# Optimization experiments

Measured on AMD Instinct MI355X. Metric: run time of the kernel, lower is better.

The kernel has to match this reference:

```python
import jax, jax.numpy as jnp
import numpy as np

B, T, F = 8192, 200, 16
H = 32  # LSTM units
D = 60  # 6 * FREQUENCY


def setup_inputs() -> dict:
    key = jax.random.key(0)
    ks = jax.random.split(key, 5)
    s = 0.1
    return {
        "x": jax.random.normal(ks[0], (B, T, F), jnp.float32),
        "W": jax.random.normal(ks[1], (F, 4 * H), jnp.float32) * s,
        "U": jax.random.normal(ks[2], (H, 4 * H), jnp.float32) * s,
        "b": jnp.zeros((4 * H,), jnp.float32),
        "W1": jax.random.normal(ks[3], (H, D), jnp.float32) * s,
        "b1": jnp.zeros((D,), jnp.float32),
        "W2": jax.random.normal(ks[4], (H, D), jnp.float32) * s,
        "b2": jnp.zeros((D,), jnp.float32),
    }


def _lstm_last(x, W, U, b):
    # Precompute input-to-gate projections for all timesteps: [B, T, 4H]
    xg = jnp.einsum('btf,fg->btg', x, W) + b
    batch = x.shape[0]
    h0 = jnp.zeros((batch, H), x.dtype)
    c0 = jnp.zeros((batch, H), x.dtype)

    def step(carry, xg_t):
        h, c = carry
        g = xg_t + h @ U  # [B, 4H]
        i, f, cc, o = jnp.split(g, 4, axis=-1)  # Keras gate order: i, f, c, o
        i = jax.nn.sigmoid(i)
        f = jax.nn.sigmoid(f)
        o = jax.nn.sigmoid(o)
        c_new = f * c + i * jax.nn.relu(cc)  # activation=relu
        h_new = o * jax.nn.relu(c_new)
        return (h_new, c_new), None

    (h_T, _), _ = jax.lax.scan(step, (h0, c0), jnp.swapaxes(xg, 0, 1))
    return h_T  # return_sequences=False -> last hidden state [B, H]


def reference(x, W, U, b, W1, b1, W2, b2):
    h = _lstm_last(x, W, U, b)
    long_pred = h @ W1 + b1
    lat_pred = h @ W2 + b2
    return (long_pred, lat_pred)
```

## Files before the change

### kernel.cpp

```cpp
#include <hip/hip_runtime.h>

#define BATCH 8192
#define TSTEPS 200
#define FEAT 16
#define HID 32
#define GATES 128
#define DOUT 60
#define ROWS 16
#define HSTRIDE 40
#define NL2E -1.44269504088896340736f

typedef __fp16 half2v __attribute__((ext_vector_type(2)));
typedef __fp16 half4v __attribute__((ext_vector_type(4)));
typedef __fp16 half8v __attribute__((ext_vector_type(8)));
typedef float  float2v __attribute__((ext_vector_type(2)));
typedef float  float4v __attribute__((ext_vector_type(4)));

__device__ __forceinline__ half2v pkrtz(float a, float b) {
    return __builtin_amdgcn_cvt_pkrtz(a, b);
}

__device__ __forceinline__ half4v pack4(float4 v) {
    half2v lo = pkrtz(v.x, v.y);
    half2v hi = pkrtz(v.z, v.w);
    half4v r;
    r[0] = lo[0]; r[1] = lo[1]; r[2] = hi[0]; r[3] = hi[1];
    return r;
}

__device__ __forceinline__ void lds_barrier() {
    __builtin_amdgcn_sched_barrier(0);
    asm volatile("s_waitcnt lgkmcnt(0)\n\ts_barrier" ::: "memory");
    __builtin_amdgcn_sched_barrier(0);
}

template <bool DO_XW, bool DO_LOAD, int LOFF>
__device__ __forceinline__ void lstm_step(
    float4& XN, const float* xp,
    const half8v (&aU)[2], const half4v (&aW)[2], const float4v (&bias)[2],
    float4v (&accx)[2], float2v& cst,
    const __fp16* hr, __fp16* hw, int hroff, int hwoff)
{
    half8v hB = *reinterpret_cast<const half8v*>(&hr[hroff]);

    float4v acc0 = __builtin_amdgcn_mfma_f32_16x16x32_f16(
        aU[0], hB, accx[0], 0, 0, 0);
    float4v acc1 = __builtin_amdgcn_mfma_f32_16x16x32_f16(
        aU[1], hB, accx[1], 0, 0, 0);

    if (DO_XW) {
        half4v ax = pack4(XN);
        accx[0] = __builtin_amdgcn_mfma_f32_16x16x16f16(
            aW[0], ax, bias[0], 0, 0, 0);
        accx[1] = __builtin_amdgcn_mfma_f32_16x16x16f16(
            aW[1], ax, bias[1], 0, 0, 0);
    }
    if (DO_LOAD)
        XN = *reinterpret_cast<const float4*>(xp + LOFF);

    const float2v one  = {1.0f, 1.0f};
    const float2v zero = {0.0f, 0.0f};
    float2v ei, ef, eo;
    ei[0] = __builtin_amdgcn_exp2f(acc0[0]);
    ei[1] = __builtin_amdgcn_exp2f(acc0[1]);
    ef[0] = __builtin_amdgcn_exp2f(acc0[2]);
    ef[1] = __builtin_amdgcn_exp2f(acc0[3]);
    eo[0] = __builtin_amdgcn_exp2f(acc1[2]);
    eo[1] = __builtin_amdgcn_exp2f(acc1[3]);
    float2v di  = one + ei;
    float2v df  = one + ef;
    float2v dov = one + eo;
    float2v cc2 = {acc1[0], acc1[1]};
    float2v rc  = __builtin_elementwise_max(cc2, zero);
    float2v num = __builtin_elementwise_fma(cst, di, rc * df);
    float2v ee  = (di * df) * dov;
    float   Q   = __builtin_amdgcn_rcpf(ee[0] * ee[1]);
    float2v ie  = {Q * ee[1], Q * ee[0]};
    float2v c2  = num * (ie * dov);
    cst = c2;
    float2v h2  = __builtin_elementwise_max(num, zero) * ie;
    *reinterpret_cast<half2v*>(&hw[hwoff]) = pkrtz(h2[0], h2[1]);

    lds_barrier();
}

__global__ __launch_bounds__(256, 1) void lstm_mfma(
    const float* __restrict__ x,
    const float* __restrict__ W,
    const float* __restrict__ U,
    const float* __restrict__ bg,
    const float* __restrict__ W1,
    const float* __restrict__ b1,
    const float* __restrict__ W2,
    const float* __restrict__ b2,
    float* __restrict__ out)
{
    const int tid  = threadIdx.x;
    const int lane = tid & 63;
    const int w    = tid >> 6;
    const int n16  = lane & 15;
    const int g    = lane >> 4;
    const int b0   = blockIdx.x * ROWS;

    __shared__ __align__(16) __fp16 hbuf[2][ROWS * HSTRIDE];

    half8v  aU[2];
    half4v  aW[2];
    float4v bias[2];
    #pragma unroll
    for (int tt2 = 0; tt2 < 2; tt2++) {
        const int gA   = 2 * tt2 + ((n16 >> 1) & 1);
        const float sA = (gA == 2) ? 1.0f : NL2E;
        const int colA = 32 * gA + 8 * w + 2 * (n16 >> 2) + (n16 & 1);
        half8v u8;
        #pragma unroll
        for (int j = 0; j < 8; j++)
            u8[j] = (__fp16)(U[(8 * g + j) * GATES + colA] * sA);
        aU[tt2] = u8;
        half4v w4;
        #pragma unroll
        for (int j = 0; j < 4; j++)
            w4[j] = (__fp16)(W[(4 * g + j) * GATES + colA] * sA);
        aW[tt2] = w4;
        float4v bv;
        #pragma unroll
        for (int r = 0; r < 4; r++) {
            const int gi = 2 * tt2 + (r >> 1);
            const int cb = 32 * gi + 8 * w + 2 * g + (r & 1);
            bv[r] = bg[cb] * ((gi == 2) ? 1.0f : NL2E);
        }
        bias[tt2] = bv;
    }

    for (int i = tid; i < ROWS * HSTRIDE; i += 256) hbuf[0][i] = (__fp16)0.f;

    const float* xrow = x + (size_t)(b0 + n16) * TSTEPS * FEAT + 4 * g;

    float4 xf0 = *reinterpret_cast<const float4*>(xrow + FEAT);
    float4 xf1 = *reinterpret_cast<const float4*>(xrow + 2 * FEAT);

    float4v accx[2];
    {
        half4v a0 = pack4(*reinterpret_cast<const float4*>(xrow));
        accx[0] = __builtin_amdgcn_mfma_f32_16x16x16f16(
            aW[0], a0, bias[0], 0, 0, 0);
        accx[1] = __builtin_amdgcn_mfma_f32_16x16x16f16(
            aW[1], a0, bias[1], 0, 0, 0);
    }

    float2v cst = {0.f, 0.f};
    const int hroff = n16 * HSTRIDE + 8 * g;
    const int hwoff = n16 * HSTRIDE + 8 * w + 2 * g;

    __syncthreads();

    const float* xp = xrow;
    for (int it = 0; it < (TSTEPS - 4) / 2; ++it) {
        lstm_step<true, true, 3 * FEAT>(xf0, xp, aU, aW, bias, accx, cst,
                                        hbuf[0], hbuf[1], hroff, hwoff);
        lstm_step<true, true, 4 * FEAT>(xf1, xp, aU, aW, bias, accx, cst,
                                        hbuf[1], hbuf[0], hroff, hwoff);
        xp += 2 * FEAT;
    }
    lstm_step<true, true, 3 * FEAT>(xf0, xp, aU, aW, bias, accx, cst,
                                    hbuf[0], hbuf[1], hroff, hwoff);
    lstm_step<true, false, 0>(xf1, xp, aU, aW, bias, accx, cst,
                              hbuf[1], hbuf[0], hroff, hwoff);
    lstm_step<true, false, 0>(xf0, xp, aU, aW, bias, accx, cst,
                              hbuf[0], hbuf[1], hroff, hwoff);
    lstm_step<false, false, 0>(xf1, xp, aU, aW, bias, accx, cst,
                               hbuf[1], hbuf[0], hroff, hwoff);

    const __fp16* hf = &hbuf[0][0];
    for (int idx = tid; idx < ROWS * DOUT; idx += 256) {
        const int row = idx / DOUT;
        const int d   = idx - row * DOUT;
        float s1 = b1[d], s2 = b2[d];
        #pragma unroll 8
        for (int k = 0; k < HID; k++) {
            float hv = (float)hf[row * HSTRIDE + k];
            s1 = fmaf(hv, W1[k * DOUT + d], s1);
            s2 = fmaf(hv, W2[k * DOUT + d], s2);
        }
        out[(size_t)(b0 + row) * DOUT + d] = s1;
        out[(size_t)BATCH * DOUT + (size_t)(b0 + row) * DOUT + d] = s2;
    }
}

extern "C" void kernel_launch(void* const* d_in, const int* in_sizes, int n_in,
                              void* d_out, int out_size, void* d_ws, size_t ws_size,
                              hipStream_t stream) {
    const float* x  = (const float*)d_in[0];
    const float* W  = (const float*)d_in[1];
    const float* U  = (const float*)d_in[2];
    const float* bg = (const float*)d_in[3];
    const float* W1 = (const float*)d_in[4];
    const float* b1 = (const float*)d_in[5];
    const float* W2 = (const float*)d_in[6];
    const float* b2 = (const float*)d_in[7];
    float* out = (float*)d_out;

    dim3 grid(BATCH / ROWS);
    dim3 block(256);
    lstm_mfma<<<grid, block, 0, stream>>>(x, W, U, bg, W1, b1, W2, b2, out);
}
```

Before: 210.0 us.

## Split gate columns across eight wavefronts with one MFMA tile each

Doubles the block to 512 threads (8 waves) so each wave owns 16 gate columns (four hidden units across i/f/c/o) and issues a single recurrent MFMA and a single input MFMA per step instead of two. Each lane now computes one hidden unit's gate math rather than two, which shortens the per-step serial dependency chain inside a wave. The cost is twice as many waves synchronising on the per-step LDS barrier, scalar fp16 LDS writes, and more threads resident per block, which may limit how many blocks share a CU.

```diff
diff --git a/kernel.cpp b/kernel.cpp
--- a/kernel.cpp
+++ b/kernel.cpp
@@ -13,7 +13,6 @@
 typedef __fp16 half2v __attribute__((ext_vector_type(2)));
 typedef __fp16 half4v __attribute__((ext_vector_type(4)));
 typedef __fp16 half8v __attribute__((ext_vector_type(8)));
-typedef float  float2v __attribute__((ext_vector_type(2)));
 typedef float  float4v __attribute__((ext_vector_type(4)));
 
 __device__ __forceinline__ half2v pkrtz(float a, float b) {
@@ -37,54 +36,40 @@
 template <bool DO_XW, bool DO_LOAD, int LOFF>
 __device__ __forceinline__ void lstm_step(
     float4& XN, const float* xp,
-    const half8v (&aU)[2], const half4v (&aW)[2], const float4v (&bias)[2],
-    float4v (&accx)[2], float2v& cst,
+    const half8v& aU, const half4v& aW, const float4v& bias,
+    float4v& accx, float& cst,
     const __fp16* hr, __fp16* hw, int hroff, int hwoff)
 {
     half8v hB = *reinterpret_cast<const half8v*>(&hr[hroff]);
 
-    float4v acc0 = __builtin_amdgcn_mfma_f32_16x16x32_f16(
-        aU[0], hB, accx[0], 0, 0, 0);
-    float4v acc1 = __builtin_amdgcn_mfma_f32_16x16x32_f16(
-        aU[1], hB, accx[1], 0, 0, 0);
+    float4v acc = __builtin_amdgcn_mfma_f32_16x16x32_f16(
+        aU, hB, accx, 0, 0, 0);
 
     if (DO_XW) {
         half4v ax = pack4(XN);
-        accx[0] = __builtin_amdgcn_mfma_f32_16x16x16f16(
-            aW[0], ax, bias[0], 0, 0, 0);
-        accx[1] = __builtin_amdgcn_mfma_f32_16x16x16f16(
-            aW[1], ax, bias[1], 0, 0, 0);
+        accx = __builtin_amdgcn_mfma_f32_16x16x16f16(aW, ax, bias, 0, 0, 0);
     }
     if (DO_LOAD)
         XN = *reinterpret_cast<const float4*>(xp + LOFF);
 
-    const float2v one  = {1.0f, 1.0f};
-    const float2v zero = {0.0f, 0.0f};
-    float2v ei, ef, eo;
-    ei[0] = __builtin_amdgcn_exp2f(acc0[0]);
-    ei[1] = __builtin_amdgcn_exp2f(acc0[1]);
-    ef[0] = __builtin_amdgcn_exp2f(acc0[2]);
-    ef[1] = __builtin_amdgcn_exp2f(acc0[3]);
-    eo[0] = __builtin_amdgcn_exp2f(acc1[2]);
-    eo[1] = __builtin_amdgcn_exp2f(acc1[3]);
-    float2v di  = one + ei;
-    float2v df  = one + ef;
-    float2v dov = one + eo;
-    float2v cc2 = {acc1[0], acc1[1]};
-    float2v rc  = __builtin_elementwise_max(cc2, zero);
-    float2v num = __builtin_elementwise_fma(cst, di, rc * df);
-    float2v ee  = (di * df) * dov;
-    float   Q   = __builtin_amdgcn_rcpf(ee[0] * ee[1]);
-    float2v ie  = {Q * ee[1], Q * ee[0]};
-    float2v c2  = num * (ie * dov);
-    cst = c2;
-    float2v h2  = __builtin_elementwise_max(num, zero) * ie;
-    *reinterpret_cast<half2v*>(&hw[hwoff]) = pkrtz(h2[0], h2[1]);
+    float ei = __builtin_amdgcn_exp2f(acc[0]);
+    float ef = __builtin_amdgcn_exp2f(acc[1]);
+    float eo = __builtin_amdgcn_exp2f(acc[3]);
+    float di  = 1.0f + ei;
+    float df  = 1.0f + ef;
+    float dov = 1.0f + eo;
+    float rc  = fmaxf(acc[2], 0.0f);
+    float num = fmaf(cst, di, rc * df);
+    float ee  = (di * df) * dov;
+    float ie  = __builtin_amdgcn_rcpf(ee);
+    cst = num * (ie * dov);
+    float h = fmaxf(num, 0.0f) * ie;
+    hw[hwoff] = (__fp16)h;
 
     lds_barrier();
 }
 
-__global__ __launch_bounds__(256, 1) void lstm_mfma(
+__global__ __launch_bounds__(512, 1) void lstm_mfma(
     const float* __restrict__ x,
     const float* __restrict__ W,
     const float* __restrict__ U,
@@ -104,53 +89,40 @@
 
     __shared__ __align__(16) __fp16 hbuf[2][ROWS * HSTRIDE];
 
-    half8v  aU[2];
-    half4v  aW[2];
-    float4v bias[2];
-    #pragma unroll
-    for (int tt2 = 0; tt2 < 2; tt2++) {
-        const int gA   = 2 * tt2 + ((n16 >> 1) & 1);
+    half8v  aU;
+    half4v  aW;
+    float4v bias;
+    {
+        const int gA   = n16 & 3;
         const float sA = (gA == 2) ? 1.0f : NL2E;
-        const int colA = 32 * gA + 8 * w + 2 * (n16 >> 2) + (n16 & 1);
-        half8v u8;
+        const int colA = 32 * gA + 4 * w + (n16 >> 2);
         #pragma unroll
         for (int j = 0; j < 8; j++)
-            u8[j] = (__fp16)(U[(8 * g + j) * GATES + colA] * sA);
-        aU[tt2] = u8;
-        half4v w4;
+            aU[j] = (__fp16)(U[(8 * g + j) * GATES + colA] * sA);
         #pragma unroll
         for (int j = 0; j < 4; j++)
-            w4[j] = (__fp16)(W[(4 * g + j) * GATES + colA] * sA);
-        aW[tt2] = w4;
-        float4v bv;
+            aW[j] = (__fp16)(W[(4 * g + j) * GATES + colA] * sA);
         #pragma unroll
-        for (int r = 0; r < 4; r++) {
-            const int gi = 2 * tt2 + (r >> 1);
-            const int cb = 32 * gi + 8 * w + 2 * g + (r & 1);
-            bv[r] = bg[cb] * ((gi == 2) ? 1.0f : NL2E);
-        }
-        bias[tt2] = bv;
+        for (int r = 0; r < 4; r++)
+            bias[r] = bg[32 * r + 4 * w + g] * ((r == 2) ? 1.0f : NL2E);
     }
 
-    for (int i = tid; i < ROWS * HSTRIDE; i += 256) hbuf[0][i] = (__fp16)0.f;
+    for (int i = tid; i < ROWS * HSTRIDE; i += 512) hbuf[0][i] = (__fp16)0.f;
 
     const float* xrow = x + (size_t)(b0 + n16) * TSTEPS * FEAT + 4 * g;
 
     float4 xf0 = *reinterpret_cast<const float4*>(xrow + FEAT);
     float4 xf1 = *reinterpret_cast<const float4*>(xrow + 2 * FEAT);
 
-    float4v accx[2];
+    float4v accx;
     {
         half4v a0 = pack4(*reinterpret_cast<const float4*>(xrow));
-        accx[0] = __builtin_amdgcn_mfma_f32_16x16x16f16(
-            aW[0], a0, bias[0], 0, 0, 0);
-        accx[1] = __builtin_amdgcn_mfma_f32_16x16x16f16(
-            aW[1], a0, bias[1], 0, 0, 0);
+        accx = __builtin_amdgcn_mfma_f32_16x16x16f16(aW, a0, bias, 0, 0, 0);
     }
 
-    float2v cst = {0.f, 0.f};
+    float cst = 0.f;
     const int hroff = n16 * HSTRIDE + 8 * g;
-    const int hwoff = n16 * HSTRIDE + 8 * w + 2 * g;
+    const int hwoff = n16 * HSTRIDE + 4 * w + g;
 
     __syncthreads();
 
@@ -172,7 +144,7 @@
                                hbuf[1], hbuf[0], hroff, hwoff);
 
     const __fp16* hf = &hbuf[0][0];
-    for (int idx = tid; idx < ROWS * DOUT; idx += 256) {
+    for (int idx = tid; idx < ROWS * DOUT; idx += 512) {
         const int row = idx / DOUT;
         const int d   = idx - row * DOUT;
         float s1 = b1[d], s2 = b2[d];
@@ -201,6 +173,6 @@
     float* out = (float*)d_out;
 
     dim3 grid(BATCH / ROWS);
-    dim3 block(256);
+    dim3 block(512);
     lstm_mfma<<<grid, block, 0, stream>>>(x, W, U, bg, W1, b1, W2, b2, out);
 }
```

New measurement: 222.6 us. 1.06x slower.

## Interleave two independent 16-row batch tiles per block to hide recurrence latency

Applied to the files above, without the earlier changes.

Each block now processes two independent 16-row LSTM groups, issuing MFMAs and epilogues for both before a single shared barrier per timestep. This is meant to fill the latency of the serial recurrence chain (MFMA to activations to LDS write to barrier) with independent work, and to halve the number of barriers per row. The grid shrinks to 256 blocks, which is roughly one per CU on MI355X, so fewer waves are resident and register pressure per thread goes up.

```diff
diff --git a/kernel.cpp b/kernel.cpp
--- a/kernel.cpp
+++ b/kernel.cpp
@@ -34,30 +34,10 @@
     __builtin_amdgcn_sched_barrier(0);
 }
 
-template <bool DO_XW, bool DO_LOAD, int LOFF>
-__device__ __forceinline__ void lstm_step(
-    float4& XN, const float* xp,
-    const half8v (&aU)[2], const half4v (&aW)[2], const float4v (&bias)[2],
-    float4v (&accx)[2], float2v& cst,
-    const __fp16* hr, __fp16* hw, int hroff, int hwoff)
+__device__ __forceinline__ void epi(
+    const float4v& acc0, const float4v& acc1, float2v& cst,
+    __fp16* hw, int hwoff)
 {
-    half8v hB = *reinterpret_cast<const half8v*>(&hr[hroff]);
-
-    float4v acc0 = __builtin_amdgcn_mfma_f32_16x16x32_f16(
-        aU[0], hB, accx[0], 0, 0, 0);
-    float4v acc1 = __builtin_amdgcn_mfma_f32_16x16x32_f16(
-        aU[1], hB, accx[1], 0, 0, 0);
-
-    if (DO_XW) {
-        half4v ax = pack4(XN);
-        accx[0] = __builtin_amdgcn_mfma_f32_16x16x16f16(
-            aW[0], ax, bias[0], 0, 0, 0);
-        accx[1] = __builtin_amdgcn_mfma_f32_16x16x16f16(
-            aW[1], ax, bias[1], 0, 0, 0);
-    }
-    if (DO_LOAD)
-        XN = *reinterpret_cast<const float4*>(xp + LOFF);
-
     const float2v one  = {1.0f, 1.0f};
     const float2v zero = {0.0f, 0.0f};
     float2v ei, ef, eo;
@@ -76,10 +56,50 @@
     float2v ee  = (di * df) * dov;
     float   Q   = __builtin_amdgcn_rcpf(ee[0] * ee[1]);
     float2v ie  = {Q * ee[1], Q * ee[0]};
-    float2v c2  = num * (ie * dov);
-    cst = c2;
+    cst = num * (ie * dov);
     float2v h2  = __builtin_elementwise_max(num, zero) * ie;
     *reinterpret_cast<half2v*>(&hw[hwoff]) = pkrtz(h2[0], h2[1]);
+}
+
+template <bool DO_XW, bool DO_LOAD, int LOFF>
+__device__ __forceinline__ void lstm_step2(
+    float4& XNa, float4& XNb, const float* xpa, const float* xpb,
+    const half8v (&aU)[2], const half4v (&aW)[2], const float4v (&bias)[2],
+    float4v (&accxA)[2], float4v (&accxB)[2], float2v& cstA, float2v& cstB,
+    const __fp16* hrA, __fp16* hwA, const __fp16* hrB, __fp16* hwB,
+    int hroff, int hwoff)
+{
+    half8v hA = *reinterpret_cast<const half8v*>(&hrA[hroff]);
+    half8v hB = *reinterpret_cast<const half8v*>(&hrB[hroff]);
+
+    float4v accA0 = __builtin_amdgcn_mfma_f32_16x16x32_f16(
+        aU[0], hA, accxA[0], 0, 0, 0);
+    float4v accA1 = __builtin_amdgcn_mfma_f32_16x16x32_f16(
+        aU[1], hA, accxA[1], 0, 0, 0);
+    float4v accB0 = __builtin_amdgcn_mfma_f32_16x16x32_f16(
+        aU[0], hB, accxB[0], 0, 0, 0);
+    float4v accB1 = __builtin_amdgcn_mfma_f32_16x16x32_f16(
+        aU[1], hB, accxB[1], 0, 0, 0);
+
+    if (DO_XW) {
+        half4v axA = pack4(XNa);
+        half4v axB = pack4(XNb);
+        accxA[0] = __builtin_amdgcn_mfma_f32_16x16x16f16(
+            aW[0], axA, bias[0], 0, 0, 0);
+        accxA[1] = __builtin_amdgcn_mfma_f32_16x16x16f16(
+            aW[1], axA, bias[1], 0, 0, 0);
+        accxB[0] = __builtin_amdgcn_mfma_f32_16x16x16f16(
+            aW[0], axB, bias[0], 0, 0, 0);
+        accxB[1] = __builtin_amdgcn_mfma_f32_16x16x16f16(
+            aW[1], axB, bias[1], 0, 0, 0);
+    }
+    if (DO_LOAD) {
+        XNa = *reinterpret_cast<const float4*>(xpa + LOFF);
+        XNb = *reinterpret_cast<const float4*>(xpb + LOFF);
+    }
+
+    epi(accA0, accA1, cstA, hwA, hwoff);
+    epi(accB0, accB1, cstB, hwB, hwoff);
 
     lds_barrier();
 }
@@ -100,9 +120,9 @@
     const int w    = tid >> 6;
     const int n16  = lane & 15;
     const int g    = lane >> 4;
-    const int b0   = blockIdx.x * ROWS;
-
-    __shared__ __align__(16) __fp16 hbuf[2][ROWS * HSTRIDE];
+    const int b0   = blockIdx.x * (2 * ROWS);
+
+    __shared__ __align__(16) __fp16 hbuf[2][2][ROWS * HSTRIDE];
 
     half8v  aU[2];
     half4v  aW[2];
@@ -132,53 +152,70 @@
         bias[tt2] = bv;
     }
 
-    for (int i = tid; i < ROWS * HSTRIDE; i += 256) hbuf[0][i] = (__fp16)0.f;
-
-    const float* xrow = x + (size_t)(b0 + n16) * TSTEPS * FEAT + 4 * g;
-
-    float4 xf0 = *reinterpret_cast<const float4*>(xrow + FEAT);
-    float4 xf1 = *reinterpret_cast<const float4*>(xrow + 2 * FEAT);
-
-    float4v accx[2];
+    for (int i = tid; i < 2 * ROWS * HSTRIDE; i += 256)
+        hbuf[0][0][i] = (__fp16)0.f;
+
+    const float* xrowA = x + (size_t)(b0 + n16) * TSTEPS * FEAT + 4 * g;
+    const float* xrowB = x + (size_t)(b0 + ROWS + n16) * TSTEPS * FEAT + 4 * g;
+
+    float4 xa0 = *reinterpret_cast<const float4*>(xrowA + FEAT);
+    float4 xa1 = *reinterpret_cast<const float4*>(xrowA + 2 * FEAT);
+    float4 xb0 = *reinterpret_cast<const float4*>(xrowB + FEAT);
+    float4 xb1 = *reinterpret_cast<const float4*>(xrowB + 2 * FEAT);
+
+    float4v accxA[2], accxB[2];
     {
-        half4v a0 = pack4(*reinterpret_cast<const float4*>(xrow));
-        accx[0] = __builtin_amdgcn_mfma_f32_16x16x16f16(
+        half4v a0 = pack4(*reinterpret_cast<const float4*>(xrowA));
+        half4v b0v = pack4(*reinterpret_cast<const float4*>(xrowB));
+        accxA[0] = __builtin_amdgcn_mfma_f32_16x16x16f16(
             aW[0], a0, bias[0], 0, 0, 0);
-        accx[1] = __builtin_amdgcn_mfma_f32_16x16x16f16(
+        accxA[1] = __builtin_amdgcn_mfma_f32_16x16x16f16(
             aW[1], a0, bias[1], 0, 0, 0);
-    }
-
-    float2v cst = {0.f, 0.f};
+        accxB[0] = __builtin_amdgcn_mfma_f32_16x16x16f16(
+            aW[0], b0v, bias[0], 0, 0, 0);
+        accxB[1] = __builtin_amdgcn_mfma_f32_16x16x16f16(
+            aW[1], b0v, bias[1], 0, 0, 0);
+    }
+
+    float2v cstA = {0.f, 0.f}, cstB = {0.f, 0.f};
     const int hroff = n16 * HSTRIDE + 8 * g;
     const int hwoff = n16 * HSTRIDE + 8 * w + 2 * g;
 
     __syncthreads();
 
-    const float* xp = xrow;
+    const float* xpa = xrowA;
+    const float* xpb = xrowB;
     for (int it = 0; it < (TSTEPS - 4) / 2; ++it) {
-        lstm_step<true, true, 3 * FEAT>(xf0, xp, aU, aW, bias, accx, cst,
-                                        hbuf[0], hbuf[1], hroff, hwoff);
-        lstm_step<true, true, 4 * FEAT>(xf1, xp, aU, aW, bias, accx, cst,
-                                        hbuf[1], hbuf[0], hroff, hwoff);
-        xp += 2 * FEAT;
-    }
-    lstm_step<true, true, 3 * FEAT>(xf0, xp, aU, aW, bias, accx, cst,
-                                    hbuf[0], hbuf[1], hroff, hwoff);
-    lstm_step<true, false, 0>(xf1, xp, aU, aW, bias, accx, cst,
-                              hbuf[1], hbuf[0], hroff, hwoff);
-    lstm_step<true, false, 0>(xf0, xp, aU, aW, bias, accx, cst,
-                              hbuf[0], hbuf[1], hroff, hwoff);
-    lstm_step<false, false, 0>(xf1, xp, aU, aW, bias, accx, cst,
-                               hbuf[1], hbuf[0], hroff, hwoff);
-
-    const __fp16* hf = &hbuf[0][0];
-    for (int idx = tid; idx < ROWS * DOUT; idx += 256) {
+        lstm_step2<true, true, 3 * FEAT>(xa0, xb0, xpa, xpb, aU, aW, bias,
+            accxA, accxB, cstA, cstB,
+            hbuf[0][0], hbuf[1][0], hbuf[0][1], hbuf[1][1], hroff, hwoff);
+        lstm_step2<true, true, 4 * FEAT>(xa1, xb1, xpa, xpb, aU, aW, bias,
+            accxA, accxB, cstA, cstB,
+            hbuf[1][0], hbuf[0][0], hbuf[1][1], hbuf[0][1], hroff, hwoff);
+        xpa += 2 * FEAT;
+        xpb += 2 * FEAT;
+    }
+    lstm_step2<true, true, 3 * FEAT>(xa0, xb0, xpa, xpb, aU, aW, bias,
+        accxA, accxB, cstA, cstB,
+        hbuf[0][0], hbuf[1][0], hbuf[0][1], hbuf[1][1], hroff, hwoff);
+    lstm_step2<true, false, 0>(xa1, xb1, xpa, xpb, aU, aW, bias,
+        accxA, accxB, cstA, cstB,
+        hbuf[1][0], hbuf[0][0], hbuf[1][1], hbuf[0][1], hroff, hwoff);
+    lstm_step2<true, false, 0>(xa0, xb0, xpa, xpb, aU, aW, bias,
+        accxA, accxB, cstA, cstB,
+        hbuf[0][0], hbuf[1][0], hbuf[0][1], hbuf[1][1], hroff, hwoff);
+    lstm_step2<false, false, 0>(xa1, xb1, xpa, xpb, aU, aW, bias,
+        accxA, accxB, cstA, cstB,
+        hbuf[1][0], hbuf[0][0], hbuf[1][1], hbuf[0][1], hroff, hwoff);
+
+    for (int idx = tid; idx < 2 * ROWS * DOUT; idx += 256) {
         const int row = idx / DOUT;
         const int d   = idx - row * DOUT;
+        const __fp16* hf = &hbuf[0][row >> 4][(row & 15) * HSTRIDE];
         float s1 = b1[d], s2 = b2[d];
         #pragma unroll 8
         for (int k = 0; k < HID; k++) {
-            float hv = (float)hf[row * HSTRIDE + k];
+            float hv = (float)hf[k];
             s1 = fmaf(hv, W1[k * DOUT + d], s1);
             s2 = fmaf(hv, W2[k * DOUT + d], s2);
         }
@@ -200,7 +237,7 @@
     const float* b2 = (const float*)d_in[7];
     float* out = (float*)d_out;
 
-    dim3 grid(BATCH / ROWS);
+    dim3 grid(BATCH / (2 * ROWS));
     dim3 block(256);
     lstm_mfma<<<grid, block, 0, stream>>>(x, W, U, bg, W1, b1, W2, b2, out);
 }
```

Result: slower. 246.6 us (+17.4%).
